# Performance work log

Hardware: AMD Instinct MI355X
Metric: run time of the kernel (lower is better)

The kernel has to match this reference:

```python
import jax, jax.numpy as jnp
import numpy as np

H = 4           # attention heads
NEG_SLOPE = 0.2 # GATConv default leaky_relu slope
BN_EPS = 1e-5


def gat_conv(x, src, dst, W, a_src, a_dst, b, N):
    # PyG GATConv (concat=True, add_self_loops=True): self-loops appended by caller.
    C = W.shape[1] // H
    h = (x @ W).reshape(N, H, C)                      # [N,H,C]
    al_s = jnp.einsum('nhc,hc->nh', h, a_src)          # [N,H]
    al_d = jnp.einsum('nhc,hc->nh', h, a_dst)
    e = jax.nn.leaky_relu(al_s[src] + al_d[dst], NEG_SLOPE)   # [E,H]
    m = jax.ops.segment_max(e, dst, num_segments=N)            # per-dst softmax (stable)
    p = jnp.exp(e - m[dst])
    s = jax.ops.segment_sum(p, dst, num_segments=N)
    alpha = p / s[dst]                                          # [E,H]
    out = jax.ops.segment_sum(alpha[:, :, None] * h[src], dst, num_segments=N)  # [N,H,C]
    return out.reshape(N, H * C) + b


def mp_layer(x, src, dst, gw, gas, gad, gb, fw, fb, fg, fbeta, N):
    gat_out = gat_conv(x, src, dst, gw, gas, gad, gb, N)
    # feature_transform: Linear -> BatchNorm1d (eval: running_mean=0, running_var=1) -> ReLU
    y = x @ fw + fb
    y = y * (fg / jnp.sqrt(1.0 + BN_EPS)) + fbeta
    y = jax.nn.relu(y)
    return gat_out + y


def forward(x, edge_index, edge_attr, params):
    N = x.shape[0]
    loop = jnp.arange(N, dtype=edge_index.dtype)
    src = jnp.concatenate([edge_index[0], loop])   # add self loops (GATConv default)
    dst = jnp.concatenate([edge_index[1], loop])
    for p in params[:-1]:
        x = mp_layer(x, src, dst, *p, N)
        x = jax.nn.relu(x)   # dropout is identity in eval mode
    cw, cb = params[-1]
    return x @ cw + cb


def setup_inputs() -> dict:
    N, E, D, Hd, O = 80000, 1000000, 512, 128, 10
    key = jax.random.key(0)
    ks = jax.random.split(key, 40)
    ki = iter(range(40))

    def rn(shape, fan_in):
        return jax.random.normal(ks[next(ki)], shape, dtype=jnp.float32) / np.sqrt(fan_in)

    inp = {}
    inp['x'] = jax.random.normal(ks[next(ki)], (N, D), dtype=jnp.float32)
    inp['edge_index'] = jax.random.randint(ks[next(ki)], (2, E), 0, N, dtype=jnp.int64)
    inp['edge_attr'] = jax.random.uniform(ks[next(ki)], (E, 1), dtype=jnp.float32)
    dims = [D, Hd, Hd]
    for li, din in enumerate(dims):
        inp[f'l{li}_gw'] = rn((din, Hd), din)
        inp[f'l{li}_gas'] = rn((H, Hd // H), Hd // H)
        inp[f'l{li}_gad'] = rn((H, Hd // H), Hd // H)
        inp[f'l{li}_gb'] = jnp.zeros((Hd,), jnp.float32)
        inp[f'l{li}_fw'] = rn((din, Hd), din)
        inp[f'l{li}_fb'] = jnp.zeros((Hd,), jnp.float32)
        inp[f'l{li}_fg'] = jnp.ones((Hd,), jnp.float32)
        inp[f'l{li}_fbeta'] = jnp.zeros((Hd,), jnp.float32)
    inp['cls_w'] = rn((Hd, O), Hd)
    inp['cls_b'] = jnp.zeros((O,), jnp.float32)
    return inp


def reference(x, edge_index, edge_attr,
              l0_gw, l0_gas, l0_gad, l0_gb, l0_fw, l0_fb, l0_fg, l0_fbeta,
              l1_gw, l1_gas, l1_gad, l1_gb, l1_fw, l1_fb, l1_fg, l1_fbeta,
              l2_gw, l2_gas, l2_gad, l2_gb, l2_fw, l2_fb, l2_fg, l2_fbeta,
              cls_w, cls_b):
    params = [
        (l0_gw, l0_gas, l0_gad, l0_gb, l0_fw, l0_fb, l0_fg, l0_fbeta),
        (l1_gw, l1_gas, l1_gad, l1_gb, l1_fw, l1_fb, l1_fg, l1_fbeta),
        (l2_gw, l2_gas, l2_gad, l2_gb, l2_fw, l2_fb, l2_fg, l2_fbeta),
        (cls_w, cls_b),
    ]
    return forward(x, edge_index, edge_attr, params)
```

## Files before the change

kernel.cpp:

```cpp
#include <hip/hip_runtime.h>
#include <cstdint>
#include <cstddef>

#define HD 128
#define NEG_SLOPE 0.2f
#define BN_EPS 1e-5f

typedef __bf16 bf16x8 __attribute__((ext_vector_type(8)));
typedef float  f32x4  __attribute__((ext_vector_type(4)));

__device__ __forceinline__ unsigned short f2b(float f) {
    unsigned int u = __float_as_uint(f);
    u = (u + 0x7fffu + ((u >> 16) & 1u)) >> 16;
    return (unsigned short)u;
}
__device__ __forceinline__ unsigned int pack2(float lo, float hi) {
    return (unsigned int)f2b(lo) | ((unsigned int)f2b(hi) << 16);
}

__global__ void prep_w2(const float* __restrict__ gw, const float* __restrict__ fw,
                        unsigned short* __restrict__ Wt, int K)
{
    int t = blockIdx.x * 256 + threadIdx.x;
    if (t >= K * 256) return;
    int k = t >> 8, c = t & 255;
    float v = (c < 128) ? gw[(size_t)k * 128 + c] : fw[(size_t)k * 128 + (c - 128)];
    Wt[(size_t)c * K + k] = f2b(v);
}

#define GLOAD(OFF)                                                            \
    pa0 = *(const float4*)(xrow + (OFF));                                     \
    pa1 = *(const float4*)(xrow + (OFF) + 4);                                 \
    pb0 = *(const uint4*)(wrow + (OFF));                                      \
    pb1 = *(const uint4*)(wrow + (OFF) + 8);

#define DSWR(BUF)                                                             \
    {                                                                         \
        uint4 av;                                                             \
        av.x = pack2(pa0.x, pa0.y); av.y = pack2(pa0.z, pa0.w);               \
        av.z = pack2(pa1.x, pa1.y); av.w = pack2(pa1.z, pa1.w);               \
        *(uint4*)((BUF) + aw)              = av;                              \
        *(uint4*)((BUF) + 10240 + bw)      = pb0;                             \
        *(uint4*)((BUF) + 10240 + bw + 16) = pb1;                             \
    }

#define COMPUTE(BUF)                                                          \
    {                                                                         \
        bf16x8 af[4], bfr[4];                                                 \
        _Pragma("unroll") for (int rt = 0; rt < 4; rt++)                      \
            af[rt] = *(const bf16x8*)((BUF) + (64 * wm + rt * 16 + m) * 80 + q * 16); \
        _Pragma("unroll") for (int ct = 0; ct < 4; ct++)                      \
            bfr[ct] = *(const bf16x8*)((BUF) + 10240 + (64 * wn + ct * 16 + m) * 80 + q * 16); \
        _Pragma("unroll") for (int rt = 0; rt < 4; rt++)                      \
            _Pragma("unroll") for (int ct = 0; ct < 4; ct++)                  \
                acc[rt][ct] = __builtin_amdgcn_mfma_f32_16x16x32_bf16(        \
                    af[rt], bfr[ct], acc[rt][ct], 0, 0, 0);                   \
    }

__global__ __launch_bounds__(512, 4) void gemm_dual(
    const float* __restrict__ X, const unsigned short* __restrict__ Wt,
    unsigned short* __restrict__ hb, float* __restrict__ yb, int M, int K,
    const float* __restrict__ fb, const float* __restrict__ fg,
    const float* __restrict__ fbeta, const float* __restrict__ gb)
{
    __shared__ __align__(16) char smem[2 * 30720];
    char* buf0 = smem;
    char* buf1 = smem + 30720;

    const int tid  = threadIdx.x;
    const int row0 = blockIdx.x * 128;
    const int w    = tid >> 6, lane = tid & 63;
    const int wm   = w & 1,  wn = w >> 1;
    const int m    = lane & 15, q = lane >> 4;

    const int ra = tid >> 2, ka = (tid & 3) * 8;
    const int rb = tid >> 1, kb = (tid & 1) * 16;

    int arow = row0 + ra; if (arow >= M) arow = M - 1;

    f32x4 acc[4][4];
#pragma unroll
    for (int rt = 0; rt < 4; rt++)
#pragma unroll
        for (int ct = 0; ct < 4; ct++) acc[rt][ct] = (f32x4){0.f, 0.f, 0.f, 0.f};

    const int aw = ra * 80 + ka * 2;
    const int bw = rb * 80 + kb * 2;

    const float* xrow = X + (size_t)arow * K + ka;
    const unsigned short* wrow = Wt + (size_t)rb * K + kb;

    float4 pa0, pa1;
    uint4  pb0, pb1;

    GLOAD(0)
    DSWR(buf0)
    __syncthreads();

    for (int ks = 0; ks < K; ks += 64) {
        GLOAD(ks + 32)
        COMPUTE(buf0)
        DSWR(buf1)
        __syncthreads();
        if (ks + 64 < K) { GLOAD(ks + 64) }
        COMPUTE(buf1)
        if (ks + 64 < K) { DSWR(buf0) }
        __syncthreads();
    }

    const bool full = (row0 + 128 <= M);
    if (wn < 2) {
#pragma unroll
        for (int ct = 0; ct < 4; ct++) {
            int col = 64 * wn + ct * 16 + m;
#pragma unroll
            for (int rt = 0; rt < 4; rt++)
#pragma unroll
                for (int r = 0; r < 4; r++) {
                    int row = row0 + 64 * wm + rt * 16 + q * 4 + r;
                    if (full || row < M) hb[(size_t)row * HD + col] = f2b(acc[rt][ct][r]);
                }
        }
    } else {
        const float inv_bn = 1.0f / sqrtf(1.0f + BN_EPS);
#pragma unroll
        for (int ct = 0; ct < 4; ct++) {
            int col = 64 * (wn - 2) + ct * 16 + m;
            float g  = fg[col] * inv_bn;
            float bb = fb[col];
            float bt = fbeta[col];
            float gv = gb[col];
#pragma unroll
            for (int rt = 0; rt < 4; rt++)
#pragma unroll
                for (int r = 0; r < 4; r++) {
                    int row = row0 + 64 * wm + rt * 16 + q * 4 + r;
                    if (full || row < M) {
                        float y = (acc[rt][ct][r] + bb) * g + bt;
                        y = y > 0.f ? y : 0.f;
                        yb[(size_t)row * HD + col] = y + gv;
                    }
                }
        }
    }
}

__global__ void al_kernel(const unsigned short* __restrict__ h,
                          const float* __restrict__ a_src, const float* __restrict__ a_dst,
                          float* __restrict__ als, float* __restrict__ ald, int N)
{
    int t = blockIdx.x * blockDim.x + threadIdx.x;
    if (t >= N * 4) return;
    int n = t >> 2, hd = t & 3;
    const unsigned short* hp = h + (size_t)n * HD + hd * 32;
    const float* as = a_src + hd * 32;
    const float* ad = a_dst + hd * 32;
    float s1 = 0.f, s2 = 0.f;
#pragma unroll
    for (int i = 0; i < 32; i += 8) {
        uint4 hv = *(const uint4*)(hp + i);
        unsigned int u[4] = {hv.x, hv.y, hv.z, hv.w};
#pragma unroll
        for (int p = 0; p < 4; p++) {
            float f0 = __uint_as_float(u[p] << 16);
            float f1 = __uint_as_float(u[p] & 0xffff0000u);
            s1 += f0 * as[i + 2 * p] + f1 * as[i + 2 * p + 1];
            s2 += f0 * ad[i + 2 * p] + f1 * ad[i + 2 * p + 1];
        }
    }
    als[t] = s1; ald[t] = s2;
}

__global__ void hist_kernel(const int* __restrict__ ei, int E, int N, int* __restrict__ deg)
{
    int t = blockIdx.x * blockDim.x + threadIdx.x;
    if (t >= E + N) return;
    int d = (t < E) ? ei[E + t] : (t - E);
    atomicAdd(&deg[d], 1);
}

__global__ void scan1(const int* __restrict__ deg, int* __restrict__ rp,
                      int* __restrict__ bsum, int N)
{
    __shared__ int sh[256];
    int t = threadIdx.x;
    int i0 = blockIdx.x * 1024 + t * 4;
    int v[4];
#pragma unroll
    for (int j = 0; j < 4; j++) v[j] = (i0 + j < N) ? deg[i0 + j] : 0;
    int tot = v[0] + v[1] + v[2] + v[3];
    sh[t] = tot;
    __syncthreads();
    for (int off = 1; off < 256; off <<= 1) {
        int xv = (t >= off) ? sh[t - off] : 0;
        __syncthreads();
        sh[t] += xv;
        __syncthreads();
    }
    int run = sh[t] - tot;
    if (t == 255) bsum[blockIdx.x] = sh[255];
#pragma unroll
    for (int j = 0; j < 4; j++) {
        if (i0 + j < N) rp[i0 + j] = run;
        run += v[j];
    }
}

__global__ void scan2(int* __restrict__ bsum, int nb)
{
    if (threadIdx.x == 0 && blockIdx.x == 0) {
        int run = 0;
        for (int i = 0; i < nb; i++) { int v = bsum[i]; bsum[i] = run; run += v; }
    }
}

__global__ void scan3(int* __restrict__ rp, int* __restrict__ cur,
                      const int* __restrict__ bsum, int N, int Etot)
{
    int t = blockIdx.x * blockDim.x + threadIdx.x;
    if (t < N) {
        int v = rp[t] + bsum[t >> 10];
        rp[t] = v;
        cur[t] = v;
    } else if (t == N) {
        rp[N] = Etot;
    }
}

__global__ void scatter_kernel(const int* __restrict__ ei, int E, int N,
                               int* __restrict__ cur, int* __restrict__ col)
{
    int t = blockIdx.x * blockDim.x + threadIdx.x;
    if (t >= E + N) return;
    int s, d;
    if (t < E) { s = ei[t]; d = ei[E + t]; } else { s = t - E; d = t - E; }
    int p = atomicAdd(&cur[d], 1);
    col[p] = s;
}

__global__ __launch_bounds__(256) void agg_kernel(
    const unsigned short* __restrict__ h, const float* __restrict__ als,
    const float* __restrict__ ald, const int* __restrict__ rp,
    const int* __restrict__ col, float* __restrict__ xio, int N)
{
    int wid  = (blockIdx.x * blockDim.x + threadIdx.x) >> 6;
    int lane = threadIdx.x & 63;
    if (wid >= N) return;
    int beg = rp[wid], end = rp[wid + 1];

    int g = lane >> 4, c = lane & 15, hB = c >> 2;
    float ad_h = ald[wid * 4 + hB];
    float acc[8];
#pragma unroll
    for (int p = 0; p < 8; p++) acc[p] = 0.f;
    float wsum = 0.f;
    const unsigned short* hbase = h + c * 8;

    int j = beg + g;
    float alc = 0.f;
    uint4 hvc = (uint4){0, 0, 0, 0};
    if (j < end) {
        int s0 = col[j];
        alc = als[s0 * 4 + hB];
        hvc = *(const uint4*)(hbase + (size_t)s0 * HD);
    }
    while (j < end) {
        int jn = j + 4;
        float aln = 0.f;
        uint4 hvn = (uint4){0, 0, 0, 0};
        if (jn < end) {
            int sn = col[jn];
            aln = als[sn * 4 + hB];
            hvn = *(const uint4*)(hbase + (size_t)sn * HD);
        }
        float e = alc + ad_h;
        e = e > 0.f ? e : NEG_SLOPE * e;
        float wgt = __expf(e);
        wsum += wgt;
        unsigned int uu[4] = {hvc.x, hvc.y, hvc.z, hvc.w};
#pragma unroll
        for (int p = 0; p < 4; p++) {
            acc[2 * p]     += wgt * __uint_as_float(uu[p] << 16);
            acc[2 * p + 1] += wgt * __uint_as_float(uu[p] & 0xffff0000u);
        }
        j = jn; alc = aln; hvc = hvn;
    }
#pragma unroll
    for (int p = 0; p < 8; p++) {
        acc[p] += __shfl_xor(acc[p], 16);
        acc[p] += __shfl_xor(acc[p], 32);
    }
    wsum += __shfl_xor(wsum, 16);
    wsum += __shfl_xor(wsum, 32);
    if (g == 0) {
        float inv = 1.0f / wsum;
        float* xp = xio + (size_t)wid * HD + c * 8;
        float4 x0 = *(float4*)xp, x1 = *(float4*)(xp + 4);
        float o[8] = {acc[0] * inv + x0.x, acc[1] * inv + x0.y,
                      acc[2] * inv + x0.z, acc[3] * inv + x0.w,
                      acc[4] * inv + x1.x, acc[5] * inv + x1.y,
                      acc[6] * inv + x1.z, acc[7] * inv + x1.w};
#pragma unroll
        for (int p = 0; p < 8; p++) o[p] = o[p] > 0.f ? o[p] : 0.f;
        *(float4*)xp       = (float4){o[0], o[1], o[2], o[3]};
        *(float4*)(xp + 4) = (float4){o[4], o[5], o[6], o[7]};
    }
}

__global__ __launch_bounds__(256) void cls_kernel(
    const float* __restrict__ x, const float* __restrict__ w,
    const float* __restrict__ b, float* __restrict__ out, int N)
{
    int wid  = (blockIdx.x * blockDim.x + threadIdx.x) >> 6;
    int lane = threadIdx.x & 63;
    if (wid >= N) return;
    float x0 = x[(size_t)wid * HD + lane];
    float x1 = x[(size_t)wid * HD + 64 + lane];
    float acc[10];
#pragma unroll
    for (int o = 0; o < 10; o++)
        acc[o] = x0 * w[lane * 10 + o] + x1 * w[(lane + 64) * 10 + o];
#pragma unroll
    for (int o = 0; o < 10; o++) {
        float v = acc[o];
#pragma unroll
        for (int off = 1; off < 64; off <<= 1) v += __shfl_xor(v, off);
        acc[o] = v;
    }
    float v = 0.f;
#pragma unroll
    for (int o = 0; o < 10; o++) if (lane == o) v = acc[o];
    if (lane < 10) out[(size_t)wid * 10 + lane] = v + b[lane];
}

extern "C" void kernel_launch(void* const* d_in, const int* in_sizes, int n_in,
                              void* d_out, int out_size, void* d_ws, size_t ws_size,
                              hipStream_t stream)
{
    const float* x0 = (const float*)d_in[0];
    const int*   ei = (const int*)d_in[1];
    const int N = in_sizes[0] / 512;
    const int E = in_sizes[1] / 2;
    const int Etot = E + N;

    const float *gw[3], *gas[3], *gad[3], *gbp[3], *fw[3], *fbp[3], *fgp[3], *fbt[3];
    for (int l = 0; l < 3; l++) {
        int b = 3 + 8 * l;
        gw[l]  = (const float*)d_in[b + 0];
        gas[l] = (const float*)d_in[b + 1];
        gad[l] = (const float*)d_in[b + 2];
        gbp[l] = (const float*)d_in[b + 3];
        fw[l]  = (const float*)d_in[b + 4];
        fbp[l] = (const float*)d_in[b + 5];
        fgp[l] = (const float*)d_in[b + 6];
        fbt[l] = (const float*)d_in[b + 7];
    }
    const float* cw = (const float*)d_in[27];
    const float* cb = (const float*)d_in[28];

    char* p = (char*)d_ws;
    auto carve = [&](size_t bytes) -> char* {
        char* r = p; p += (bytes + 255) & ~(size_t)255; return r;
    };
    float* xA   = (float*)carve((size_t)N * HD * 4);
    float* xB   = (float*)carve((size_t)N * HD * 4);
    unsigned short* hbuf = (unsigned short*)carve((size_t)N * HD * 2);
    float* als  = (float*)carve((size_t)N * 4 * 4);
    float* ald  = (float*)carve((size_t)N * 4 * 4);
    int* rp   = (int*)carve((size_t)(N + 1) * 4);
    int* deg  = (int*)carve((size_t)N * 4);
    int* cur  = (int*)carve((size_t)N * 4);
    int* bsum = (int*)carve(4096);
    int* col  = (int*)carve((size_t)Etot * 4);
    unsigned short* wT[3];
    for (int l = 0; l < 3; l++) {
        int K = (l == 0) ? 512 : HD;
        wT[l] = (unsigned short*)carve((size_t)256 * K * 2);
    }

    for (int l = 0; l < 3; l++) {
        int K = (l == 0) ? 512 : HD;
        int nt = K * 256;
        prep_w2<<<(nt + 255) / 256, 256, 0, stream>>>(gw[l], fw[l], wT[l], K);
    }

    hipMemsetAsync(deg, 0, (size_t)N * 4, stream);
    hist_kernel<<<(Etot + 255) / 256, 256, 0, stream>>>(ei, E, N, deg);
    int nb = (N + 1023) / 1024;
    scan1<<<nb, 256, 0, stream>>>(deg, rp, bsum, N);
    scan2<<<1, 64, 0, stream>>>(bsum, nb);
    scan3<<<(N + 256) / 256, 256, 0, stream>>>(rp, cur, bsum, N, Etot);
    scatter_kernel<<<(Etot + 255) / 256, 256, 0, stream>>>(ei, E, N, cur, col);

    for (int l = 0; l < 3; l++) {
        const float* xin = (l == 0) ? x0 : ((l == 1) ? xA : xB);
        float* xout = (l == 1) ? xB : xA;
        int K = (l == 0) ? 512 : HD;
        int mblocks = (N + 127) / 128;
        gemm_dual<<<mblocks, 512, 0, stream>>>(xin, wT[l], hbuf, xout, N, K,
                                               fbp[l], fgp[l], fbt[l], gbp[l]);
        al_kernel<<<(N * 4 + 255) / 256, 256, 0, stream>>>(hbuf, gas[l], gad[l], als, ald, N);
        agg_kernel<<<(N + 3) / 4, 256, 0, stream>>>(hbuf, als, ald, rp, col, xout, N);
    }

    cls_kernel<<<(N + 3) / 4, 256, 0, stream>>>(xA, cw, cb, (float*)d_out, N);
}
```

Baseline: 776.5 us.

## Stage GEMM tiles via direct global-to-LDS loads with swizzled layout

The dual GEMM now loads A (fp32) and B (bf16) tiles straight from global memory into LDS with global_load_lds, instead of going through registers. It uses XOR-swizzled layouts to avoid bank conflicts and explicit vmcnt waits plus barriers to pipeline the double buffer. The fp32-to-bf16 conversion of X moves from the store path to the LDS read path, so each wave repeats it per fragment. This frees registers and cuts VGPR traffic, but LDS use grows to 64KB per block, which could reduce occupancy.

```diff
diff --git a/kernel.cpp b/kernel.cpp
--- a/kernel.cpp
+++ b/kernel.cpp
@@ -16,6 +16,12 @@
 }
 __device__ __forceinline__ unsigned int pack2(float lo, float hi) {
     return (unsigned int)f2b(lo) | ((unsigned int)f2b(hi) << 16);
+}
+
+__device__ __forceinline__ void gload_lds16(const void* g, void* l) {
+    __builtin_amdgcn_global_load_lds(
+        (const __attribute__((address_space(1))) uint32_t*)g,
+        (__attribute__((address_space(3))) uint32_t*)l, 16, 0, 0);
 }
 
 __global__ void prep_w2(const float* __restrict__ gw, const float* __restrict__ fw,
@@ -28,29 +34,35 @@
     Wt[(size_t)c * K + k] = f2b(v);
 }
 
-#define GLOAD(OFF)                                                            \
-    pa0 = *(const float4*)(xrow + (OFF));                                     \
-    pa1 = *(const float4*)(xrow + (OFF) + 4);                                 \
-    pb0 = *(const uint4*)(wrow + (OFF));                                      \
-    pb1 = *(const uint4*)(wrow + (OFF) + 8);
-
-#define DSWR(BUF)                                                             \
-    {                                                                         \
-        uint4 av;                                                             \
-        av.x = pack2(pa0.x, pa0.y); av.y = pack2(pa0.z, pa0.w);               \
-        av.z = pack2(pa1.x, pa1.y); av.w = pack2(pa1.z, pa1.w);               \
-        *(uint4*)((BUF) + aw)              = av;                              \
-        *(uint4*)((BUF) + 10240 + bw)      = pb0;                             \
-        *(uint4*)((BUF) + 10240 + bw + 16) = pb1;                             \
-    }
+#define WAITV4 asm volatile("s_waitcnt vmcnt(4)" ::: "memory");
+#define WAITV0 asm volatile("s_waitcnt vmcnt(0)" ::: "memory");
+#define BAR    __builtin_amdgcn_s_barrier();
+
+#define STAGE(BUF, KOFF)                                                      \
+    _Pragma("unroll") for (int i = 0; i < 2; i++)                             \
+        gload_lds16(ap[i] + (KOFF), (BUF) + (w + i * 8) * 1024);              \
+    _Pragma("unroll") for (int i = 0; i < 2; i++)                             \
+        gload_lds16(bp[i] + (KOFF), (BUF) + 16384 + (w + i * 8) * 1024);
 
 #define COMPUTE(BUF)                                                          \
     {                                                                         \
         bf16x8 af[4], bfr[4];                                                 \
-        _Pragma("unroll") for (int rt = 0; rt < 4; rt++)                      \
-            af[rt] = *(const bf16x8*)((BUF) + (64 * wm + rt * 16 + m) * 80 + q * 16); \
-        _Pragma("unroll") for (int ct = 0; ct < 4; ct++)                      \
-            bfr[ct] = *(const bf16x8*)((BUF) + 10240 + (64 * wn + ct * 16 + m) * 80 + q * 16); \
+        _Pragma("unroll") for (int rt = 0; rt < 4; rt++) {                    \
+            int arow = 64 * wm + rt * 16 + m;                                 \
+            const char* base = (BUF) + (arow << 7);                           \
+            int sw = (m & 7) << 4;                                            \
+            f32x4 a0 = *(const f32x4*)(base + ((q * 32)      ^ sw));          \
+            f32x4 a1 = *(const f32x4*)(base + ((q * 32 + 16) ^ sw));          \
+            uint4 av;                                                         \
+            av.x = pack2(a0.x, a0.y); av.y = pack2(a0.z, a0.w);               \
+            av.z = pack2(a1.x, a1.y); av.w = pack2(a1.z, a1.w);               \
+            af[rt] = *(bf16x8*)&av;                                           \
+        }                                                                     \
+        _Pragma("unroll") for (int ct = 0; ct < 4; ct++) {                    \
+            int brow = 64 * wn + ct * 16 + m;                                 \
+            bfr[ct] = *(const bf16x8*)((BUF) + 16384 + (brow << 6) +          \
+                                       ((q * 16) ^ (((m >> 1) & 3) << 4)));   \
+        }                                                                     \
         _Pragma("unroll") for (int rt = 0; rt < 4; rt++)                      \
             _Pragma("unroll") for (int ct = 0; ct < 4; ct++)                  \
                 acc[rt][ct] = __builtin_amdgcn_mfma_f32_16x16x32_bf16(        \
@@ -63,9 +75,9 @@
     const float* __restrict__ fb, const float* __restrict__ fg,
     const float* __restrict__ fbeta, const float* __restrict__ gb)
 {
-    __shared__ __align__(16) char smem[2 * 30720];
+    __shared__ __align__(16) char smem[2 * 32768];
     char* buf0 = smem;
-    char* buf1 = smem + 30720;
+    char* buf1 = smem + 32768;
 
     const int tid  = threadIdx.x;
     const int row0 = blockIdx.x * 128;
@@ -73,10 +85,21 @@
     const int wm   = w & 1,  wn = w >> 1;
     const int m    = lane & 15, q = lane >> 4;
 
-    const int ra = tid >> 2, ka = (tid & 3) * 8;
-    const int rb = tid >> 1, kb = (tid & 1) * 16;
-
-    int arow = row0 + ra; if (arow >= M) arow = M - 1;
+    const int la = lane >> 3, ca = lane & 7;
+    const int lb = lane >> 2, cb = lane & 3;
+    const int oA = 4 * (ca ^ la);
+    const int oB = 8 * (cb ^ (la & 3));
+
+    const float* ap[2];
+    const unsigned short* bp[2];
+#pragma unroll
+    for (int i = 0; i < 2; i++) {
+        int ch = w + i * 8;
+        int gr = row0 + ch * 8 + la; if (gr >= M) gr = M - 1;
+        ap[i] = X + (size_t)gr * K + oA;
+        int rB = ch * 16 + lb;
+        bp[i] = Wt + (size_t)rB * K + oB;
+    }
 
     f32x4 acc[4][4];
 #pragma unroll
@@ -84,28 +107,17 @@
 #pragma unroll
         for (int ct = 0; ct < 4; ct++) acc[rt][ct] = (f32x4){0.f, 0.f, 0.f, 0.f};
 
-    const int aw = ra * 80 + ka * 2;
-    const int bw = rb * 80 + kb * 2;
-
-    const float* xrow = X + (size_t)arow * K + ka;
-    const unsigned short* wrow = Wt + (size_t)rb * K + kb;
-
-    float4 pa0, pa1;
-    uint4  pb0, pb1;
-
-    GLOAD(0)
-    DSWR(buf0)
-    __syncthreads();
-
+    STAGE(buf0, 0)
     for (int ks = 0; ks < K; ks += 64) {
-        GLOAD(ks + 32)
+        STAGE(buf1, ks + 32)
+        WAITV4
+        BAR
         COMPUTE(buf0)
-        DSWR(buf1)
-        __syncthreads();
-        if (ks + 64 < K) { GLOAD(ks + 64) }
+        BAR
+        if (ks + 64 < K) { STAGE(buf0, ks + 64) WAITV4 } else { WAITV0 }
+        BAR
         COMPUTE(buf1)
-        if (ks + 64 < K) { DSWR(buf0) }
-        __syncthreads();
+        BAR
     }
 
     const bool full = (row0 + 128 <= M);
```

After: 770.8 us. Within noise of the previous version (-0.7%).
